# Kernel tuning notes

Measured on AMD Instinct MI355X. Metric: run time of the kernel, lower is better.

## Reference

```python
import jax, jax.numpy as jnp
import numpy as np
from jax import lax

CHUNK = 128
EPS = 1e-6


def rmsnorm(x, w, eps=EPS):
    var = jnp.mean(jnp.square(x.astype(jnp.float32)), axis=-1, keepdims=True)
    return (x * lax.rsqrt(var + eps)).astype(x.dtype) * w


def linear_attn(q, k, v, slopes):
    """Decay-based (lightning/RetNet-style) causal linear attention.
    q,k,v: [B,H,S,D]; slopes: [H,1,1] positive per-head decay rates.
    out[i] = sum_{j<=i} exp(-s*(i-j)) * (q_i . k_j) * v_j, via chunked scan.
    """
    B, H, S, D = q.shape
    C = CHUNK
    nC = S // C
    s = slopes.reshape(1, H, 1, 1).astype(jnp.float32)  # [1,H,1,1]
    t = jnp.arange(C, dtype=jnp.float32)
    q_dec = jnp.exp(-s * t[None, None, :, None])            # [1,H,C,1] decay for inter-chunk query
    k_dec = jnp.exp(-s * (C - t)[None, None, :, None])      # [1,H,C,1] decay applied to keys entering state
    chunk_dec = jnp.exp(-s * C)                              # [1,H,1,1] whole-chunk state decay
    rel = t[:, None] - t[None, :]                            # [C,C]
    intra_dec = jnp.where(rel >= 0, jnp.exp(-s * rel), 0.0)  # [1,H,C,C] causal intra-chunk decay

    # [nC,B,H,C,D]
    qc = q.reshape(B, H, nC, C, D).transpose(2, 0, 1, 3, 4)
    kc = k.reshape(B, H, nC, C, D).transpose(2, 0, 1, 3, 4)
    vc = v.reshape(B, H, nC, C, D).transpose(2, 0, 1, 3, 4)

    def step(kv, inp):
        qi, ki, vi = inp  # each [B,H,C,D]; kv: [B,H,D,D]
        inter = jnp.einsum('bhcd,bhde->bhce', qi * q_dec, kv)
        scores = jnp.einsum('bhcd,bhed->bhce', qi, ki) * intra_dec  # [B,H,C,C]
        intra = jnp.einsum('bhce,bhed->bhcd', scores, vi)
        kv_new = chunk_dec * kv + jnp.einsum('bhcd,bhce->bhde', ki * k_dec, vi)
        return kv_new, inter + intra

    kv0 = jnp.zeros((B, H, D, D), dtype=jnp.float32)
    _, out = lax.scan(step, kv0, (qc, kc, vc))  # out: [nC,B,H,C,D]
    return out.transpose(1, 2, 0, 3, 4).reshape(B, H, S, D)


def setup_inputs() -> dict:
    key = jax.random.key(0)
    ks = jax.random.split(key, 8)
    B, S, E, H, D = 2, 2048, 2048, 16, 128
    init = 0.02
    hidden_states = jax.random.normal(ks[0], (B, S, E), dtype=jnp.float32)
    attention_mask = jnp.ones((B, S), dtype=jnp.float32)
    # standard ALiBi-like per-head slopes in (0,1]
    slope_rate = (2.0 ** (-8.0 * (jnp.arange(H, dtype=jnp.float32) + 1.0) / H)).reshape(H, 1, 1)
    Wq = jax.random.normal(ks[1], (E, H * D), dtype=jnp.float32) * init
    Wk = jax.random.normal(ks[2], (E, H * D), dtype=jnp.float32) * init
    Wv = jax.random.normal(ks[3], (E, H * D), dtype=jnp.float32) * init
    Wg = jax.random.normal(ks[4], (E, H * D), dtype=jnp.float32) * init
    Wo = jax.random.normal(ks[5], (H * D, E), dtype=jnp.float32) * init
    norm_w = jnp.ones((H * D,), dtype=jnp.float32)
    return {"hidden_states": hidden_states, "attention_mask": attention_mask,
            "slope_rate": slope_rate, "Wq": Wq, "Wk": Wk, "Wv": Wv,
            "Wg": Wg, "Wo": Wo, "norm_w": norm_w}


def reference(hidden_states, attention_mask, slope_rate, Wq, Wk, Wv, Wg, Wo, norm_w):
    B, S, E = hidden_states.shape
    H = slope_rate.shape[0]
    D = Wq.shape[1] // H
    q = (hidden_states @ Wq).reshape(B, S, H, D).transpose(0, 2, 1, 3)
    k = (hidden_states @ Wk).reshape(B, S, H, D).transpose(0, 2, 1, 3)
    v = (hidden_states @ Wv).reshape(B, S, H, D).transpose(0, 2, 1, 3)
    v = v * attention_mask[:, None, :, None]
    out = linear_attn(q, k, v, slope_rate)                      # [B,H,S,D]
    out = out.transpose(0, 2, 1, 3).reshape(B, S, H * D)        # b h n d -> b n (h d)
    out = rmsnorm(out, norm_w)
    out = jax.nn.sigmoid(hidden_states @ Wg) * out
    return out @ Wo
```

## Files before the change

kernel.cpp:

```cpp
#include <hip/hip_runtime.h>
#include <cstdint>
#include <cstddef>

typedef unsigned short u16;
typedef unsigned int   u32;

#define SEQ    2048
#define EDIM   2048
#define HEADS  16
#define DHEAD  128
#define CCH    128
#define NCH    16
#define TOKENS 4096

typedef __attribute__((ext_vector_type(8))) short short8;
typedef __attribute__((ext_vector_type(4))) float floatx4;

__device__ __forceinline__ float b2f(u16 b) {
    u32 u = ((u32)b) << 16; float f; __builtin_memcpy(&f, &u, 4); return f;
}
__device__ __forceinline__ u16 f2b(float f) {
    u32 u; __builtin_memcpy(&u, &f, 4);
    u32 r = (u + 0x7fffu + ((u >> 16) & 1u)) >> 16;
    return (u16)r;
}
__device__ __forceinline__ void unpack8(uint4 u, float* f) {
    f[0] = b2f((u16)(u.x & 0xffff)); f[1] = b2f((u16)(u.x >> 16));
    f[2] = b2f((u16)(u.y & 0xffff)); f[3] = b2f((u16)(u.y >> 16));
    f[4] = b2f((u16)(u.z & 0xffff)); f[5] = b2f((u16)(u.z >> 16));
    f[6] = b2f((u16)(u.w & 0xffff)); f[7] = b2f((u16)(u.w >> 16));
}
__device__ __forceinline__ uint4 pack8(const float* f) {
    uint4 u;
    u.x = (u32)f2b(f[0]) | ((u32)f2b(f[1]) << 16);
    u.y = (u32)f2b(f[2]) | ((u32)f2b(f[3]) << 16);
    u.z = (u32)f2b(f[4]) | ((u32)f2b(f[5]) << 16);
    u.w = (u32)f2b(f[6]) | ((u32)f2b(f[7]) << 16);
    return u;
}

__device__ __forceinline__ void gld_lds16(const u16* g, u16* l) {
    __builtin_amdgcn_global_load_lds((const __attribute__((address_space(1))) void*)g,
                                     (__attribute__((address_space(3))) void*)l, 16, 0, 0);
}
#define CFENCE() __asm__ volatile("" ::: "memory")
#define RAW_BARRIER() do { CFENCE(); __builtin_amdgcn_s_barrier(); CFENCE(); } while (0)

__global__ __launch_bounds__(256) void k_f32_to_bf16(const float* __restrict__ in,
                                                     u16* __restrict__ out) {
    int i = blockIdx.x * 256 + threadIdx.x;
    float4 v = ((const float4*)in)[i];
    uint2 o;
    o.x = (u32)f2b(v.x) | ((u32)f2b(v.y) << 16);
    o.y = (u32)f2b(v.z) | ((u32)f2b(v.w) << 16);
    ((uint2*)out)[i] = o;
}

__global__ void k_transW(const float* __restrict__ W0, const float* __restrict__ W1,
                         const float* __restrict__ W2, const float* __restrict__ W3,
                         const float* __restrict__ W4, u16* __restrict__ out) {
    const float* W;
    int z = blockIdx.z;
    switch (z) {
        case 0: W = W0; break; case 1: W = W1; break; case 2: W = W2; break;
        case 3: W = W3; break; default: W = W4; break;
    }
    __shared__ float tile[32][33];
    int n = blockIdx.x * 32 + threadIdx.x;
    int k = blockIdx.y * 32 + threadIdx.y;
    tile[threadIdx.y][threadIdx.x] = W[(size_t)k * EDIM + n];
    __syncthreads();
    int on = blockIdx.x * 32 + threadIdx.y;
    int ok = blockIdx.y * 32 + threadIdx.x;
    out[(size_t)z * EDIM * EDIM + (size_t)on * EDIM + ok] = f2b(tile[threadIdx.x][threadIdx.y]);
}

__global__ __launch_bounds__(256, 4) void k_gemm(const u16* __restrict__ A,
                                                 const u16* __restrict__ Bt,
                                                 void* __restrict__ C,
                                                 int K, int N,
                                                 long long zstrB, long long zstrC,
                                                 int out_bf16, int mode,
                                                 u16* __restrict__ KdT,
                                                 u16* __restrict__ VT,
                                                 const float* __restrict__ slopes,
                                                 const float* __restrict__ mask) {
    __shared__ u16 As[2][128 * 32];
    __shared__ u16 Bs[2][128 * 32];
    int z = blockIdx.z;
    const u16* Bz = Bt + (size_t)z * (size_t)zstrB;
    int m0 = blockIdx.y * 128, n0 = blockIdx.x * 128;
    int tid = threadIdx.x;
    int w = tid >> 6, lane = tid & 63;
    int wr = w >> 1, wc = w & 1;
    int lrow = lane & 15, khalf = lane >> 4;

    floatx4 acc[4][4];
#pragma unroll
    for (int i = 0; i < 4; i++)
#pragma unroll
        for (int j = 0; j < 4; j++) acc[i][j] = (floatx4){0.f, 0.f, 0.f, 0.f};

    const u16* aptr[2];
    const u16* bptr[2];
    int loff[2];
#pragma unroll
    for (int i = 0; i < 2; i++) {
        int c = tid + i * 256;
        int row = c >> 2, slot = c & 3;
        int g = slot ^ ((row >> 1) & 3);
        aptr[i] = A  + (size_t)(m0 + row) * K + g * 8;
        bptr[i] = Bz + (size_t)(n0 + row) * K + g * 8;
        loff[i] = c * 8;
    }
    int aoff[4], boff[4];
#pragma unroll
    for (int i = 0; i < 4; i++) {
        int ra = wr * 64 + i * 16 + lrow;
        int rb = wc * 64 + i * 16 + lrow;
        aoff[i] = ra * 32 + ((khalf ^ ((ra >> 1) & 3)) * 8);
        boff[i] = rb * 32 + ((khalf ^ ((rb >> 1) & 3)) * 8);
    }

    int nIter = K >> 5;
#pragma unroll
    for (int i = 0; i < 2; i++) gld_lds16(aptr[i] + 0,  &As[0][loff[i]]);
#pragma unroll
    for (int i = 0; i < 2; i++) gld_lds16(bptr[i] + 0,  &Bs[0][loff[i]]);
#pragma unroll
    for (int i = 0; i < 2; i++) gld_lds16(aptr[i] + 32, &As[1][loff[i]]);
#pragma unroll
    for (int i = 0; i < 2; i++) gld_lds16(bptr[i] + 32, &Bs[1][loff[i]]);

    for (int it = 0; it < nIter; ++it) {
        if (it + 1 < nIter) __builtin_amdgcn_s_waitcnt(0xF74);
        else                __builtin_amdgcn_s_waitcnt(0xF70);
        RAW_BARRIER();
        int buf = it & 1;
        short8 af[4], bfr[4];
#pragma unroll
        for (int i = 0; i < 4; i++) af[i]  = *(const short8*)&As[buf][aoff[i]];
#pragma unroll
        for (int j = 0; j < 4; j++) bfr[j] = *(const short8*)&Bs[buf][boff[j]];
#pragma unroll
        for (int i = 0; i < 4; i++)
#pragma unroll
            for (int j = 0; j < 4; j++)
                acc[i][j] = __builtin_amdgcn_mfma_f32_16x16x32_bf16(af[i], bfr[j], acc[i][j], 0, 0, 0);
        RAW_BARRIER();
        if (it + 2 < nIter) {
            int k0 = (it + 2) * 32;
#pragma unroll
            for (int i = 0; i < 2; i++) gld_lds16(aptr[i] + k0, &As[buf][loff[i]]);
#pragma unroll
            for (int i = 0; i < 2; i++) gld_lds16(bptr[i] + k0, &Bs[buf][loff[i]]);
        }
    }

    int writeVT  = (mode == 1 && z == 2);
    int writeKdT = (mode == 1 && z == 1);

    if (!writeVT) {
        size_t cz = (size_t)z * (size_t)zstrC;
#pragma unroll
        for (int i = 0; i < 4; i++)
#pragma unroll
            for (int j = 0; j < 4; j++) {
                int mrow = m0 + wr * 64 + i * 16 + khalf * 4;
                int ncol = n0 + wc * 64 + j * 16 + lrow;
#pragma unroll
                for (int r = 0; r < 4; r++) {
                    float val = acc[i][j][r];
                    if (out_bf16)
                        ((u16*)C)[cz + (size_t)(mrow + r) * N + ncol] = f2b(val);
                    else
                        ((float*)C)[cz + (size_t)(mrow + r) * N + ncol] = val;
                }
            }
    }
    if (writeVT || writeKdT) {
        int b = blockIdx.y >> 4, cc = blockIdx.y & 15, h = blockIdx.x;
        size_t tile = ((size_t)b * 256 + (size_t)h * 16 + (size_t)cc) * 16384;
        float s = slopes[h];
        u16* dst = (writeVT ? VT : KdT) + tile;
#pragma unroll
        for (int i = 0; i < 4; i++)
#pragma unroll
            for (int j = 0; j < 4; j++) {
                int t0 = wr * 64 + i * 16 + khalf * 4;
                int d  = wc * 64 + j * 16 + lrow;
                u16 pk[4];
#pragma unroll
                for (int r = 0; r < 4; r++) {
                    int t = t0 + r;
                    float sc = writeVT ? mask[(size_t)b * SEQ + cc * CCH + t]
                                       : __expf(-s * (float)(CCH - t));
                    pk[r] = f2b(acc[i][j][r] * sc);
                }
                *(uint2*)&dst[(size_t)d * 128 + t0] = *(const uint2*)pk;
            }
    }
}

__global__ __launch_bounds__(256) void k_kvc(const u16* __restrict__ VT,
                                             const u16* __restrict__ KdT,
                                             u16* __restrict__ kvT) {
    int bid = blockIdx.x, tid = threadIdx.x;
    int w = tid >> 6, lane = tid & 63;
    int wr = w >> 1, wc = w & 1;
    int lrow = lane & 15, khalf = lane >> 4;
    const u16* va = VT  + (size_t)bid * 16384;
    const u16* kb = KdT + (size_t)bid * 16384;
    floatx4 acc[4][4];
#pragma unroll
    for (int i = 0; i < 4; i++)
#pragma unroll
        for (int j = 0; j < 4; j++) acc[i][j] = (floatx4){0.f, 0.f, 0.f, 0.f};
#pragma unroll
    for (int kk = 0; kk < 4; kk++) {
        short8 a[4], bf[4];
#pragma unroll
        for (int i = 0; i < 4; i++)
            a[i] = *(const short8*)(va + (size_t)(wr * 64 + i * 16 + lrow) * 128 + kk * 32 + khalf * 8);
#pragma unroll
        for (int j = 0; j < 4; j++)
            bf[j] = *(const short8*)(kb + (size_t)(wc * 64 + j * 16 + lrow) * 128 + kk * 32 + khalf * 8);
#pragma unroll
        for (int i = 0; i < 4; i++)
#pragma unroll
            for (int j = 0; j < 4; j++)
                acc[i][j] = __builtin_amdgcn_mfma_f32_16x16x32_bf16(a[i], bf[j], acc[i][j], 0, 0, 0);
    }
    u16* o = kvT + (size_t)bid * 16384;
#pragma unroll
    for (int i = 0; i < 4; i++)
#pragma unroll
        for (int j = 0; j < 4; j++)
#pragma unroll
            for (int r = 0; r < 4; r++)
                o[(size_t)(wr * 64 + i * 16 + khalf * 4 + r) * 128 + wc * 64 + j * 16 + lrow] =
                    f2b(acc[i][j][r]);
}

__global__ __launch_bounds__(256) void k_scan(u16* __restrict__ kvbuf,
                                              const float* __restrict__ slopes) {
    int gid = blockIdx.x * 256 + threadIdx.x;
    int idx = gid & 16383;
    int bh = gid >> 14;
    int h = bh & 15;
    float cd = __expf(-slopes[h] * (float)CCH);
    u16* p = kvbuf + (size_t)bh * NCH * 16384 + idx;
    float st = 0.f;
    for (int c = 0; c < NCH; c++) {
        float tmp = b2f(p[(size_t)c * 16384]);
        p[(size_t)c * 16384] = f2b(st);
        st = cd * st + tmp;
    }
}

__global__ __launch_bounds__(256) void k_attn_out(const u16* __restrict__ q,
                                                  const u16* __restrict__ k,
                                                  const u16* __restrict__ VT,
                                                  const u16* __restrict__ kvT,
                                                  const float* __restrict__ slopes,
                                                  u16* __restrict__ attn) {
    __shared__ u16 KS[128 * 136];
    int bid = blockIdx.x;
    int c = bid & 15, h = (bid >> 4) & 15, b = bid >> 8;
    float s = slopes[h];
    int tid = threadIdx.x;
    int w = tid >> 6, lane = tid & 63;
    int wr = w >> 1, wc = w & 1;
    int lrow = lane & 15, khalf = lane >> 4;
    size_t tokbase = (size_t)(b * SEQ + c * CCH);

    {
        const u16* kg = k + tokbase * EDIM + h * DHEAD;
#pragma unroll
        for (int i = 0; i < 8; i++) {
            int cidx = tid + i * 256;
            int t = cidx >> 4, part = (cidx & 15) * 8;
            *(uint4*)&KS[t * 136 + part] = *(const uint4*)(kg + (size_t)t * EDIM + part);
        }
    }
    short8 qa[4][4];
    {
        const u16* qgbase = q + tokbase * EDIM + h * DHEAD;
#pragma unroll
        for (int i = 0; i < 4; i++) {
            const u16* qrow = qgbase + (size_t)(wr * 64 + i * 16 + lrow) * EDIM;
#pragma unroll
            for (int kk = 0; kk < 4; kk++)
                qa[i][kk] = *(const short8*)(qrow + kk * 32 + khalf * 8);
        }
    }
    __syncthreads();

    floatx4 acc[4][4];
#pragma unroll
    for (int i = 0; i < 4; i++)
#pragma unroll
        for (int j = 0; j < 4; j++) acc[i][j] = (floatx4){0.f, 0.f, 0.f, 0.f};
#pragma unroll
    for (int kk = 0; kk < 4; kk++) {
        short8 bf[4];
#pragma unroll
        for (int j = 0; j < 4; j++)
            bf[j] = *(const short8*)&KS[(wc * 64 + j * 16 + lrow) * 136 + kk * 32 + khalf * 8];
#pragma unroll
        for (int i = 0; i < 4; i++)
#pragma unroll
            for (int j = 0; j < 4; j++)
                acc[i][j] = __builtin_amdgcn_mfma_f32_16x16x32_bf16(qa[i][kk], bf[j], acc[i][j], 0, 0, 0);
    }
    __syncthreads();

#pragma unroll
    for (int i = 0; i < 4; i++)
#pragma unroll
        for (int j = 0; j < 4; j++) {
            int tbase = wr * 64 + i * 16 + khalf * 4;
            int u = wc * 64 + j * 16 + lrow;
#pragma unroll
            for (int r = 0; r < 4; r++) {
                int t = tbase + r;
                float val = (t >= u) ? acc[i][j][r] * __expf(-s * (float)(t - u)) : 0.f;
                KS[t * 136 + u] = f2b(val);
            }
        }
    __syncthreads();

#pragma unroll
    for (int i = 0; i < 4; i++)
#pragma unroll
        for (int j = 0; j < 4; j++) acc[i][j] = (floatx4){0.f, 0.f, 0.f, 0.f};
    const u16* st = kvT + (size_t)bid * 16384;
#pragma unroll
    for (int kk = 0; kk < 4; kk++) {
        short8 bf[4];
#pragma unroll
        for (int j = 0; j < 4; j++)
            bf[j] = *(const short8*)(st + (size_t)(wc * 64 + j * 16 + lrow) * 128 + kk * 32 + khalf * 8);
#pragma unroll
        for (int i = 0; i < 4; i++)
#pragma unroll
            for (int j = 0; j < 4; j++)
                acc[i][j] = __builtin_amdgcn_mfma_f32_16x16x32_bf16(qa[i][kk], bf[j], acc[i][j], 0, 0, 0);
    }
#pragma unroll
    for (int i = 0; i < 4; i++)
#pragma unroll
        for (int r = 0; r < 4; r++) {
            float qd = __expf(-s * (float)(wr * 64 + i * 16 + khalf * 4 + r));
#pragma unroll
            for (int j = 0; j < 4; j++) acc[i][j][r] *= qd;
        }
    const u16* vt = VT + (size_t)bid * 16384;
#pragma unroll
    for (int kk = 0; kk < 4; kk++) {
        short8 sa[4], bf[4];
#pragma unroll
        for (int i = 0; i < 4; i++)
            sa[i] = *(const short8*)&KS[(wr * 64 + i * 16 + lrow) * 136 + kk * 32 + khalf * 8];
#pragma unroll
        for (int j = 0; j < 4; j++)
            bf[j] = *(const short8*)(vt + (size_t)(wc * 64 + j * 16 + lrow) * 128 + kk * 32 + khalf * 8);
#pragma unroll
        for (int i = 0; i < 4; i++)
#pragma unroll
            for (int j = 0; j < 4; j++)
                acc[i][j] = __builtin_amdgcn_mfma_f32_16x16x32_bf16(sa[i], bf[j], acc[i][j], 0, 0, 0);
    }

    u16* og = attn + tokbase * EDIM + h * DHEAD;
#pragma unroll
    for (int i = 0; i < 4; i++)
#pragma unroll
        for (int j = 0; j < 4; j++)
#pragma unroll
            for (int r = 0; r < 4; r++)
                og[(size_t)(wr * 64 + i * 16 + khalf * 4 + r) * EDIM + wc * 64 + j * 16 + lrow] =
                    f2b(acc[i][j][r]);
}

__global__ __launch_bounds__(256) void k_rms_gate(const u16* __restrict__ attn,
                                                  const u16* __restrict__ gpre,
                                                  const float* __restrict__ nw,
                                                  u16* __restrict__ out) {
    int n = blockIdx.x, tid = threadIdx.x;
    float a[8];
    unpack8(((const uint4*)(attn + (size_t)n * EDIM))[tid], a);
    float ss = 0.f;
#pragma unroll
    for (int j = 0; j < 8; j++) ss += a[j] * a[j];
#pragma unroll
    for (int o = 32; o > 0; o >>= 1) ss += __shfl_down(ss, o, 64);
    __shared__ float red[5];
    int w = tid >> 6, lane = tid & 63;
    if (lane == 0) red[w] = ss;
    __syncthreads();
    if (tid == 0) red[4] = rsqrtf((red[0] + red[1] + red[2] + red[3]) / 2048.f + 1e-6f);
    __syncthreads();
    float rs = red[4];
    float g[8];
    unpack8(((const uint4*)(gpre + (size_t)n * EDIM))[tid], g);
    const float4* np4 = (const float4*)(nw + tid * 8);
    float4 w0 = np4[0], w1 = np4[1];
    float wv[8] = {w0.x, w0.y, w0.z, w0.w, w1.x, w1.y, w1.z, w1.w};
    float o8[8];
#pragma unroll
    for (int j = 0; j < 8; j++) {
        float sg = 1.f / (1.f + __expf(-g[j]));
        o8[j] = sg * (a[j] * rs * wv[j]);
    }
    ((uint4*)(out + (size_t)n * EDIM))[tid] = pack8(o8);
}

extern "C" void kernel_launch(void* const* d_in, const int* in_sizes, int n_in,
                              void* d_out, int out_size, void* d_ws, size_t ws_size,
                              hipStream_t stream) {
    const float* hs     = (const float*)d_in[0];
    const float* mask   = (const float*)d_in[1];
    const float* slopes = (const float*)d_in[2];
    const float* Wq     = (const float*)d_in[3];
    const float* Wk     = (const float*)d_in[4];
    const float* Wv     = (const float*)d_in[5];
    const float* Wg     = (const float*)d_in[6];
    const float* Wo     = (const float*)d_in[7];
    const float* nw     = (const float*)d_in[8];
    float* out = (float*)d_out;

    char* ws = (char*)d_ws;
    u16* hsb   = (u16*)ws;
    u16* Wt    = (u16*)(ws + 16777216LL);
    u16* qkvg  = (u16*)(ws + 58720256LL);
    u16* kvbuf = (u16*)(ws + 125829120LL);
    u16* attn  = (u16*)(ws + 142606336LL);
    u16* qb  = qkvg;
    u16* kb  = qkvg + 8388608LL;
    u16* VT  = qkvg + 16777216LL;
    u16* gb  = qkvg + 25165824LL;
    u16* KdT = attn;

    k_f32_to_bf16<<<8192, 256, 0, stream>>>(hs, hsb);
    k_transW<<<dim3(64, 64, 5), dim3(32, 32, 1), 0, stream>>>(Wq, Wk, Wv, Wg, Wo, Wt);
    k_gemm<<<dim3(16, 32, 4), 256, 0, stream>>>(hsb, Wt, qkvg, EDIM, EDIM,
                                                (long long)EDIM * EDIM,
                                                (long long)TOKENS * EDIM, 1,
                                                1, KdT, VT, slopes, mask);
    k_kvc<<<512, 256, 0, stream>>>(VT, KdT, kvbuf);
    k_scan<<<2048, 256, 0, stream>>>(kvbuf, slopes);
    k_attn_out<<<512, 256, 0, stream>>>(qb, kb, VT, kvbuf, slopes, attn);
    k_rms_gate<<<TOKENS, 256, 0, stream>>>(attn, gb, nw, hsb);
    k_gemm<<<dim3(16, 32, 1), 256, 0, stream>>>(hsb, Wt + 4LL * 4194304LL, out, EDIM, EDIM,
                                                0LL, 0LL, 0,
                                                0, (u16*)nullptr, (u16*)nullptr, slopes, mask);
}
```

Before: 439.2 us.

## Pre-swizzle weights into MFMA fragment layout and load B directly to registers

The weight transpose kernel now writes each weight matrix in a fragment-ordered layout, so every lane's 16-byte MFMA B operand is contiguous. The GEMM drops the B LDS buffers and loads B fragments straight from global memory into registers, double-buffered across iterations, with only A still staged through LDS. The aim is to halve LDS traffic and LDS usage per block, at the cost of exposing global load latency for B in registers and more register pressure, hence launch bounds lowered from 4 to 3. The waitcnt values are adjusted to track the changed count of outstanding loads.

```diff
diff --git a/kernel.cpp b/kernel.cpp
--- a/kernel.cpp
+++ b/kernel.cpp
@@ -45,6 +45,11 @@
 }
 #define CFENCE() __asm__ volatile("" ::: "memory")
 #define RAW_BARRIER() do { CFENCE(); __builtin_amdgcn_s_barrier(); CFENCE(); } while (0)
+
+__device__ __forceinline__ size_t wfrag_off(int n, int k) {
+    return (size_t)(n >> 4) * (16 * EDIM) + (size_t)(k >> 5) * 512 +
+           (size_t)(((k >> 3) & 3) * 128 + (n & 15) * 8 + (k & 7));
+}
 
 __global__ __launch_bounds__(256) void k_f32_to_bf16(const float* __restrict__ in,
                                                      u16* __restrict__ out) {
@@ -72,10 +77,37 @@
     __syncthreads();
     int on = blockIdx.x * 32 + threadIdx.y;
     int ok = blockIdx.y * 32 + threadIdx.x;
-    out[(size_t)z * EDIM * EDIM + (size_t)on * EDIM + ok] = f2b(tile[threadIdx.x][threadIdx.y]);
-}
-
-__global__ __launch_bounds__(256, 4) void k_gemm(const u16* __restrict__ A,
+    out[(size_t)z * EDIM * EDIM + wfrag_off(on, ok)] = f2b(tile[threadIdx.x][threadIdx.y]);
+}
+
+#define GEMM_STEP(IT, BUF, BCUR, BNEXT, VMC)                                    \
+  {                                                                             \
+    __builtin_amdgcn_s_waitcnt(VMC);                                            \
+    RAW_BARRIER();                                                              \
+    short8 af[4];                                                               \
+    _Pragma("unroll")                                                           \
+    for (int i = 0; i < 4; i++) af[i] = *(const short8*)&As[BUF][aoff[i]];      \
+    if ((IT) + 1 < nIter) {                                                     \
+      int kb = ((IT) + 1) * 512;                                                \
+      _Pragma("unroll")                                                         \
+      for (int j = 0; j < 4; j++)                                               \
+        BNEXT[j] = *(const short8*)(bBase[j] + kb);                             \
+    }                                                                           \
+    _Pragma("unroll")                                                           \
+    for (int i = 0; i < 4; i++)                                                 \
+      _Pragma("unroll")                                                         \
+      for (int j = 0; j < 4; j++)                                               \
+        acc[i][j] = __builtin_amdgcn_mfma_f32_16x16x32_bf16(af[i], BCUR[j],     \
+                                                            acc[i][j], 0, 0, 0);\
+    RAW_BARRIER();                                                              \
+    if ((IT) + 2 < nIter) {                                                     \
+      int k0 = ((IT) + 2) * 32;                                                 \
+      _Pragma("unroll")                                                         \
+      for (int i = 0; i < 2; i++) gld_lds16(aptr[i] + k0, &As[BUF][loffA[i]]);  \
+    }                                                                           \
+  }
+
+__global__ __launch_bounds__(256, 3) void k_gemm(const u16* __restrict__ A,
                                                  const u16* __restrict__ Bt,
                                                  void* __restrict__ C,
                                                  int K, int N,
@@ -86,7 +118,6 @@
                                                  const float* __restrict__ slopes,
                                                  const float* __restrict__ mask) {
     __shared__ u16 As[2][128 * 32];
-    __shared__ u16 Bs[2][128 * 32];
     int z = blockIdx.z;
     const u16* Bz = Bt + (size_t)z * (size_t)zstrB;
     int m0 = blockIdx.y * 128, n0 = blockIdx.x * 128;
@@ -102,60 +133,45 @@
         for (int j = 0; j < 4; j++) acc[i][j] = (floatx4){0.f, 0.f, 0.f, 0.f};
 
     const u16* aptr[2];
-    const u16* bptr[2];
-    int loff[2];
+    int loffA[2];
 #pragma unroll
     for (int i = 0; i < 2; i++) {
         int c = tid + i * 256;
         int row = c >> 2, slot = c & 3;
         int g = slot ^ ((row >> 1) & 3);
-        aptr[i] = A  + (size_t)(m0 + row) * K + g * 8;
-        bptr[i] = Bz + (size_t)(n0 + row) * K + g * 8;
-        loff[i] = c * 8;
-    }
-    int aoff[4], boff[4];
+        aptr[i] = A + (size_t)(m0 + row) * K + g * 8;
+        loffA[i] = c * 8;
+    }
+    int aoff[4];
 #pragma unroll
     for (int i = 0; i < 4; i++) {
         int ra = wr * 64 + i * 16 + lrow;
-        int rb = wc * 64 + i * 16 + lrow;
         aoff[i] = ra * 32 + ((khalf ^ ((ra >> 1) & 3)) * 8);
-        boff[i] = rb * 32 + ((khalf ^ ((rb >> 1) & 3)) * 8);
+    }
+    const u16* bBase[4];
+#pragma unroll
+    for (int j = 0; j < 4; j++) {
+        int g16 = (n0 + wc * 64 + j * 16) >> 4;
+        bBase[j] = Bz + (size_t)g16 * (16 * (size_t)K) + khalf * 128 + lrow * 8;
     }
 
     int nIter = K >> 5;
 #pragma unroll
-    for (int i = 0; i < 2; i++) gld_lds16(aptr[i] + 0,  &As[0][loff[i]]);
-#pragma unroll
-    for (int i = 0; i < 2; i++) gld_lds16(bptr[i] + 0,  &Bs[0][loff[i]]);
-#pragma unroll
-    for (int i = 0; i < 2; i++) gld_lds16(aptr[i] + 32, &As[1][loff[i]]);
-#pragma unroll
-    for (int i = 0; i < 2; i++) gld_lds16(bptr[i] + 32, &Bs[1][loff[i]]);
-
-    for (int it = 0; it < nIter; ++it) {
-        if (it + 1 < nIter) __builtin_amdgcn_s_waitcnt(0xF74);
-        else                __builtin_amdgcn_s_waitcnt(0xF70);
-        RAW_BARRIER();
-        int buf = it & 1;
-        short8 af[4], bfr[4];
-#pragma unroll
-        for (int i = 0; i < 4; i++) af[i]  = *(const short8*)&As[buf][aoff[i]];
-#pragma unroll
-        for (int j = 0; j < 4; j++) bfr[j] = *(const short8*)&Bs[buf][boff[j]];
-#pragma unroll
-        for (int i = 0; i < 4; i++)
-#pragma unroll
-            for (int j = 0; j < 4; j++)
-                acc[i][j] = __builtin_amdgcn_mfma_f32_16x16x32_bf16(af[i], bfr[j], acc[i][j], 0, 0, 0);
-        RAW_BARRIER();
-        if (it + 2 < nIter) {
-            int k0 = (it + 2) * 32;
-#pragma unroll
-            for (int i = 0; i < 2; i++) gld_lds16(aptr[i] + k0, &As[buf][loff[i]]);
-#pragma unroll
-            for (int i = 0; i < 2; i++) gld_lds16(bptr[i] + k0, &Bs[buf][loff[i]]);
-        }
-    }
+    for (int i = 0; i < 2; i++) gld_lds16(aptr[i] + 0,  &As[0][loffA[i]]);
+#pragma unroll
+    for (int i = 0; i < 2; i++) gld_lds16(aptr[i] + 32, &As[1][loffA[i]]);
+    CFENCE();
+    short8 bA[4], bB[4];
+#pragma unroll
+    for (int j = 0; j < 4; j++) bA[j] = *(const short8*)(bBase[j]);
+
+    int it = 0;
+    for (; it + 3 < nIter; it += 2) {
+        GEMM_STEP(it,     0, bA, bB, 0xF76);
+        GEMM_STEP(it + 1, 1, bB, bA, 0xF76);
+    }
+    GEMM_STEP(it,     0, bA, bB, 0xF76);
+    GEMM_STEP(it + 1, 1, bB, bA, 0xF74);
 
     int writeVT  = (mode == 1 && z == 2);
     int writeKdT = (mode == 1 && z == 1);
```

Measured after the change: 424.2 us. -3.4%, faster.
